# Optimization experiments

Measured on AMD Instinct MI355X. Metric: run time of the kernel, lower is better.

## Reference

```python
import jax, jax.numpy as jnp
import numpy as np
import math

S, B, HID = 1024, 2, 2048
NH, KVH, HDIM = 16, 4, 128
FFN, E, TOPK = 4096, 8, 2
CAP_F = 1.0
Q_PER_KV = NH // KVH
GROUP = (Q_PER_KV + 2) * HDIM
QKV_SIZE = KVH * GROUP
T = S * B
CAPACITY = max(4, int(math.ceil(TOPK * CAP_F * T / E)))
EPS = 1.1920929e-07


def _xavier(key, shape, fan_in, fan_out):
    lim = math.sqrt(6.0 / (fan_in + fan_out))
    return jax.random.uniform(key, shape, jnp.float32, -lim, lim)


def setup_inputs() -> dict:
    key = jax.random.key(0)
    ks = jax.random.split(key, 8)
    return {
        'hidden_states': jax.random.normal(ks[0], (S, B, HID), jnp.float32),
        'ln1_w': jnp.ones((HID,), jnp.float32),
        'ln1_b': jnp.zeros((HID,), jnp.float32),
        'qkv_w': _xavier(ks[1], (QKV_SIZE, HID), HID, QKV_SIZE),
        'proj_w': _xavier(ks[2], (HID, NH * HDIM), NH * HDIM, HID),
        'ln2_w': jnp.ones((HID,), jnp.float32),
        'ln2_b': jnp.zeros((HID,), jnp.float32),
        'gate_w': _xavier(ks[3], (HID, E), HID, E),
        'w1': _xavier(ks[4], (E, HID, FFN), HID, FFN),  # expert fc1 [E, HID, FFN]
        'w2': _xavier(ks[5], (E, FFN, HID), FFN, HID),  # expert fc2 [E, FFN, HID]
    }


def _layer_norm(x, w, b):
    mu = x.mean(-1, keepdims=True)
    var = ((x - mu) ** 2).mean(-1, keepdims=True)
    return (x - mu) * jax.lax.rsqrt(var + 1e-5) * w + b


def _attention(hs, ln1_w, ln1_b, qkv_w, proj_w):
    ln1 = _layer_norm(hs, ln1_w, ln1_b)
    qkv = jnp.einsum('sbh,oh->sbo', ln1, qkv_w)
    qkv = qkv.reshape(S, B, KVH, GROUP)
    q_dim = Q_PER_KV * HDIM
    q = qkv[..., :q_dim].reshape(S, B, NH, HDIM)
    k = qkv[..., q_dim:q_dim + HDIM]          # [S,B,KVH,HDIM]
    v = qkv[..., q_dim + HDIM:]               # [S,B,KVH,HDIM]
    # batch-first, GQA expand kv heads
    q_bf = q.transpose(1, 0, 2, 3)                         # [B,S,NH,HDIM]
    k_bf = jnp.repeat(k.transpose(1, 0, 2, 3), Q_PER_KV, axis=2)
    v_bf = jnp.repeat(v.transpose(1, 0, 2, 3), Q_PER_KV, axis=2)
    scale = 1.0 / math.sqrt(HDIM)
    scores = jnp.einsum('bqhd,bkhd->bhqk', q_bf, k_bf) * scale
    causal = jnp.tril(jnp.ones((S, S), bool))
    scores = jnp.where(causal, scores, jnp.finfo(scores.dtype).min)
    attn = jax.nn.softmax(scores, axis=-1)
    out = jnp.einsum('bhqk,bkhd->bqhd', attn, v_bf)        # [B,S,NH,HDIM]
    out_sp = out.transpose(1, 0, 2, 3).reshape(S, B, NH * HDIM)
    return jnp.einsum('sbo,ho->sbh', out_sp, proj_w)


def _moe(x, gate_w, w1, w2):
    # x: [T, HID]; deterministic DeepSpeed-style top-2 gating with capacity drop
    logits = jnp.einsum('th,he->te', x, gate_w)
    gates = jax.nn.softmax(logits, axis=-1)
    idx1 = jnp.argmax(gates, axis=-1)
    mask1 = jax.nn.one_hot(idx1, E, dtype=jnp.int32)
    logits2 = jnp.where(mask1.astype(bool), jnp.finfo(logits.dtype).min, logits)
    idx2 = jnp.argmax(logits2, axis=-1)
    mask2 = jax.nn.one_hot(idx2, E, dtype=jnp.int32)
    loc1 = jnp.cumsum(mask1, axis=0) - mask1                 # position within expert
    loc2 = jnp.cumsum(mask2, axis=0) - mask2 + mask1.sum(axis=0, keepdims=True)
    mask1 = mask1 * (loc1 < CAPACITY)
    mask2 = mask2 * (loc2 < CAPACITY)
    m1f = mask1.astype(gates.dtype)
    m2f = mask2.astype(gates.dtype)
    g1 = (gates * m1f).sum(-1)
    g2 = (gates * m2f).sum(-1)
    denom = jnp.maximum(g1 + g2, EPS)
    g1, g2 = g1 / denom, g2 / denom
    p1 = (loc1 * mask1).sum(-1)
    p2 = (loc2 * mask2).sum(-1)
    c1 = (g1[:, None] * m1f)[:, :, None] * jax.nn.one_hot(p1, CAPACITY, dtype=gates.dtype)[:, None, :]
    c2 = (g2[:, None] * m2f)[:, :, None] * jax.nn.one_hot(p2, CAPACITY, dtype=gates.dtype)[:, None, :]
    combine = c1 + c2                                        # [T,E,C]
    dispatch = (combine > 0).astype(x.dtype)
    xe = jnp.einsum('tec,th->ech', dispatch, x)              # [E,C,HID]
    h = jax.nn.gelu(jnp.einsum('ech,ehf->ecf', xe, w1), approximate=False)
    eo = jnp.einsum('ecf,efh->ech', h, w2)                   # [E,C,HID]
    return jnp.einsum('tec,ech->th', combine, eo)


def reference(hidden_states, ln1_w, ln1_b, qkv_w, proj_w, ln2_w, ln2_b, gate_w, w1, w2):
    h1 = hidden_states + _attention(hidden_states, ln1_w, ln1_b, qkv_w, proj_w)
    ln2 = _layer_norm(h1, ln2_w, ln2_b)
    moe_out = _moe(ln2.reshape(T, HID), gate_w, w1, w2).reshape(S, B, HID)
    return h1 + moe_out
```

## Files before the change

### kernel.cpp

```cpp
#include <hip/hip_runtime.h>
#include <math.h>

#define S_LEN 1024
#define BATCH 2
#define HIDN  2048
#define NHEAD 16
#define KVHN  4
#define HDIM  128
#define FFND  4096
#define NEXP  8
#define CAPC  512
#define TTOK  2048
#define QKVSZ 3072
#define GRP   768

#define BM  128
#define BKS 32
#define BKM 64
#define LDT 40

typedef float           f32x4 __attribute__((ext_vector_type(4)));
typedef __bf16          bf16x8 __attribute__((ext_vector_type(8)));
typedef unsigned short  u16x8 __attribute__((ext_vector_type(8)));
typedef unsigned short  u16x4 __attribute__((ext_vector_type(4)));

static __device__ __forceinline__ unsigned short f2bf(float f) {
  unsigned int u = __builtin_bit_cast(unsigned int, f);
  u += 0x7FFFu + ((u >> 16) & 1u);
  return (unsigned short)(u >> 16);
}
static __device__ __forceinline__ float bf2f(unsigned short h) {
  unsigned int u = ((unsigned int)h) << 16;
  return __builtin_bit_cast(float, u);
}
static __device__ __forceinline__ bf16x8 ldbf8(const unsigned short* p) {
  return __builtin_bit_cast(bf16x8, *(const u16x8*)p);
}
static __device__ __forceinline__ f32x4 mfma16(bf16x8 a, bf16x8 b, f32x4 c) {
  return __builtin_amdgcn_mfma_f32_16x16x32_bf16(a, b, c, 0, 0, 0);
}
static __device__ __forceinline__ void gl_lds16(const unsigned short* g, unsigned short* l) {
  __builtin_amdgcn_global_load_lds(
      (const __attribute__((address_space(1))) unsigned int*)g,
      (__attribute__((address_space(3))) unsigned int*)l, 16, 0, 0);
}

__global__ __launch_bounds__(256) void ln_kernel(
    const float* __restrict__ X, const float* __restrict__ W, const float* __restrict__ Bi,
    unsigned short* __restrict__ Yh, unsigned short* __restrict__ Yl, float* __restrict__ Yf) {
  __shared__ float red[256];
  int t = blockIdx.x, tid = threadIdx.x;
  const float* row = X + (size_t)t * HIDN;
  float x[8];
  {
    float4 a = *(const float4*)(row + tid * 8);
    float4 b = *(const float4*)(row + tid * 8 + 4);
    x[0]=a.x; x[1]=a.y; x[2]=a.z; x[3]=a.w; x[4]=b.x; x[5]=b.y; x[6]=b.z; x[7]=b.w;
  }
  float s = 0.f;
#pragma unroll
  for (int j = 0; j < 8; j++) s += x[j];
  red[tid] = s; __syncthreads();
  for (int o = 128; o > 0; o >>= 1) { if (tid < o) red[tid] += red[tid + o]; __syncthreads(); }
  float mu = red[0] * (1.0f / HIDN);
  __syncthreads();
  float ss = 0.f;
#pragma unroll
  for (int j = 0; j < 8; j++) { float d = x[j] - mu; ss += d * d; }
  red[tid] = ss; __syncthreads();
  for (int o = 128; o > 0; o >>= 1) { if (tid < o) red[tid] += red[tid + o]; __syncthreads(); }
  float var = red[0] * (1.0f / HIDN);
  float rstd = 1.0f / sqrtf(var + 1e-5f);
#pragma unroll
  for (int j = 0; j < 8; j++) {
    int hh = tid * 8 + j;
    float y = (x[j] - mu) * rstd * W[hh] + Bi[hh];
    size_t idx = (size_t)t * HIDN + hh;
    if (Yf) Yf[idx] = y;
    unsigned short hv = f2bf(y);
    Yh[idx] = hv;
    if (Yl) Yl[idx] = f2bf(y - bf2f(hv));
  }
}

__global__ __launch_bounds__(256) void wsplit(const float* __restrict__ W,
    unsigned short* __restrict__ Wh, unsigned short* __restrict__ Wl) {
  size_t i = ((size_t)blockIdx.x * 256 + threadIdx.x) * 8;
  float4 a = *(const float4*)(W + i);
  float4 b = *(const float4*)(W + i + 4);
  float v[8] = {a.x, a.y, a.z, a.w, b.x, b.y, b.z, b.w};
  u16x8 hv, lv;
#pragma unroll
  for (int j = 0; j < 8; j++) {
    unsigned short h = f2bf(v[j]);
    hv[j] = h; lv[j] = f2bf(v[j] - bf2f(h));
  }
  *(u16x8*)(Wh + i) = hv;
  *(u16x8*)(Wl + i) = lv;
}

__global__ __launch_bounds__(256) void tconv(const float* __restrict__ W,
    unsigned short* __restrict__ Wt, int K, int N) {
  __shared__ unsigned short T[64][72];
  int z = blockIdx.z;
  const float* Wz = W + (size_t)z * K * N;
  unsigned short* Oz = Wt + (size_t)z * N * K;
  int k0 = blockIdx.y * 64, n0 = blockIdx.x * 64;
  int tid = threadIdx.x;
  int kr = (tid >> 4) << 1, n4 = (tid & 15) << 2;
#pragma unroll
  for (int i = 0; i < 2; i++) {
    int k = kr + i * 32;
    float4 a = *(const float4*)(Wz + (size_t)(k0 + k) * N + n0 + n4);
    float4 b = *(const float4*)(Wz + (size_t)(k0 + k + 1) * N + n0 + n4);
    float av[4] = {a.x, a.y, a.z, a.w};
    float bv[4] = {b.x, b.y, b.z, b.w};
#pragma unroll
    for (int j = 0; j < 4; j++) {
      unsigned int pk = (unsigned int)f2bf(av[j]) | ((unsigned int)f2bf(bv[j]) << 16);
      *(unsigned int*)&T[n4 + j][k] = pk;
    }
  }
  __syncthreads();
  int nr = tid >> 3, c = (tid & 7) << 3;
#pragma unroll
  for (int r = 0; r < 2; r++) {
    int n = nr + r * 32;
    u16x8 v = *(const u16x8*)&T[n][c];
    *(u16x8*)(Oz + (size_t)(n0 + n) * K + k0 + c) = v;
  }
}

__global__ __launch_bounds__(256) void gemm_x3s(
    const unsigned short* __restrict__ Ah, const unsigned short* __restrict__ Al,
    const unsigned short* __restrict__ Bh, const unsigned short* __restrict__ Bl,
    float* __restrict__ Cp, int M, int N, int K2, int ldk) {
  __shared__ __align__(16) unsigned short sAh[2][4096], sAl[2][4096], sBh[2][4096], sBl[2][4096];
  int tid = threadIdx.x;
  int nbm = M >> 7, nbn = N >> 7, per = nbm * nbn;
  int cpx = gridDim.x >> 3;
  int bid = blockIdx.x;
  int l = (bid & 7) * cpx + (bid >> 3);
  int kh = l / per;
  int r = l % per;
  int nb = r / nbm, mb = r % nbm;
  int m0 = mb * BM, n0 = nb * BM;
  size_t ko = (size_t)kh * K2;
  int wv = tid >> 6, lane = tid & 63;
  int wr = wv >> 1, wc = wv & 1;
  int lm = lane & 15, lk = lane >> 4;
  f32x4 acc[4][4];
#pragma unroll
  for (int mi = 0; mi < 4; mi++)
#pragma unroll
    for (int ni = 0; ni < 4; ni++) { acc[mi][ni][0]=0.f; acc[mi][ni][1]=0.f; acc[mi][ni][2]=0.f; acc[mi][ni][3]=0.f; }
  int ri = lane >> 2, ccx = lane & 3;
  int swze = (ccx ^ ((ri >> 1) & 3)) * 8;
  int g0 = wv * 2, g1 = g0 + 1;
  const unsigned short* pah0 = Ah + (size_t)(m0 + g0 * 16 + ri) * ldk + ko + swze;
  const unsigned short* pah1 = Ah + (size_t)(m0 + g1 * 16 + ri) * ldk + ko + swze;
  const unsigned short* pal0 = Al + (size_t)(m0 + g0 * 16 + ri) * ldk + ko + swze;
  const unsigned short* pal1 = Al + (size_t)(m0 + g1 * 16 + ri) * ldk + ko + swze;
  const unsigned short* pbh0 = Bh + (size_t)(n0 + g0 * 16 + ri) * ldk + ko + swze;
  const unsigned short* pbh1 = Bh + (size_t)(n0 + g1 * 16 + ri) * ldk + ko + swze;
  const unsigned short* pbl0 = Bl + (size_t)(n0 + g0 * 16 + ri) * ldk + ko + swze;
  const unsigned short* pbl1 = Bl + (size_t)(n0 + g1 * 16 + ri) * ldk + ko + swze;
  int d0 = g0 * 512, d1 = g1 * 512;
  auto stage = [&](int buf, int ks) {
    gl_lds16(pah0 + ks, &sAh[buf][d0]); gl_lds16(pah1 + ks, &sAh[buf][d1]);
    gl_lds16(pal0 + ks, &sAl[buf][d0]); gl_lds16(pal1 + ks, &sAl[buf][d1]);
    gl_lds16(pbh0 + ks, &sBh[buf][d0]); gl_lds16(pbh1 + ks, &sBh[buf][d1]);
    gl_lds16(pbl0 + ks, &sBl[buf][d0]); gl_lds16(pbl1 + ks, &sBl[buf][d1]);
  };
  int nt = K2 / BKS;
  stage(0, 0);
  stage(1, BKS);
  int sa = (lk ^ ((lm >> 1) & 3)) * 8;
  for (int t = 0; t < nt; t++) {
    if (t + 1 < nt) { asm volatile("s_waitcnt vmcnt(8)" ::: "memory"); }
    else            { asm volatile("s_waitcnt vmcnt(0)" ::: "memory"); }
    __builtin_amdgcn_sched_barrier(0);
    __builtin_amdgcn_s_barrier();
    int cur = t & 1;
    bf16x8 fah[4], fal[4], fbh[4], fbl[4];
#pragma unroll
    for (int mi = 0; mi < 4; mi++) {
      int ro = (wr * 64 + mi * 16 + lm) * 32 + sa;
      fah[mi] = ldbf8(&sAh[cur][ro]); fal[mi] = ldbf8(&sAl[cur][ro]);
    }
#pragma unroll
    for (int ni = 0; ni < 4; ni++) {
      int ro = (wc * 64 + ni * 16 + lm) * 32 + sa;
      fbh[ni] = ldbf8(&sBh[cur][ro]); fbl[ni] = ldbf8(&sBl[cur][ro]);
    }
#pragma unroll
    for (int mi = 0; mi < 4; mi++)
#pragma unroll
      for (int ni = 0; ni < 4; ni++) {
        acc[mi][ni] = mfma16(fah[mi], fbh[ni], acc[mi][ni]);
        acc[mi][ni] = mfma16(fal[mi], fbh[ni], acc[mi][ni]);
        acc[mi][ni] = mfma16(fah[mi], fbl[ni], acc[mi][ni]);
      }
    __builtin_amdgcn_s_barrier();
    if (t + 2 < nt) stage(cur, (t + 2) * BKS);
  }
  float* Cslab = Cp + (size_t)kh * M * N;
#pragma unroll
  for (int mi = 0; mi < 4; mi++)
#pragma unroll
    for (int ni = 0; ni < 4; ni++)
#pragma unroll
      for (int rr = 0; rr < 4; rr++) {
        int row = m0 + wr * 64 + mi * 16 + lk * 4 + rr;
        int col = n0 + wc * 64 + ni * 16 + lm;
        Cslab[(size_t)row * N + col] = acc[mi][ni][rr];
      }
}

template<int GELU, int SPLITK>
__global__ __launch_bounds__(256) void gemm_moe(
    const unsigned short* __restrict__ A, const unsigned short* __restrict__ Bt,
    void* __restrict__ Cp, int M, int N, int K, int ld) {
  __shared__ __align__(16) unsigned short sA[2][8192], sB[2][8192];
  int tid = threadIdx.x;
  int nbm = M >> 7, nbn = N >> 7, per = nbm * nbn;
  int cpx = gridDim.x >> 3;
  int bid = blockIdx.x;
  int l = (bid & 7) * cpx + (bid >> 3);
  int z = l / per;
  int r = l % per;
  int nb = r / nbm, mb = r % nbm;
  int m0 = mb * BM, n0 = nb * BM;
  const unsigned short* Az;
  const unsigned short* Bz;
  if (SPLITK) {
    int e = z >> 1, kh = z & 1;
    Az = A + (size_t)e * M * ld + (size_t)kh * K;
    Bz = Bt + (size_t)e * N * ld + (size_t)kh * K;
  } else {
    Az = A + (size_t)z * M * ld;
    Bz = Bt + (size_t)z * N * ld;
  }
  int wv = tid >> 6, lane = tid & 63;
  int wr = wv >> 1, wc = wv & 1;
  int lm = lane & 15, lk = lane >> 4;
  f32x4 acc[4][4];
#pragma unroll
  for (int mi = 0; mi < 4; mi++)
#pragma unroll
    for (int ni = 0; ni < 4; ni++) { acc[mi][ni][0]=0.f; acc[mi][ni][1]=0.f; acc[mi][ni][2]=0.f; acc[mi][ni][3]=0.f; }
  int ri = lane >> 3, cc8 = lane & 7;
  int swze = (cc8 ^ ri) * 8;
  const unsigned short* pa[4];
  const unsigned short* pb[4];
#pragma unroll
  for (int j = 0; j < 4; j++) {
    int g = wv * 4 + j;
    pa[j] = Az + (size_t)(m0 + g * 8 + ri) * ld + swze;
    pb[j] = Bz + (size_t)(n0 + g * 8 + ri) * ld + swze;
  }
  int dbase = wv * 4 * 512;
  auto stage = [&](int buf, int ks) {
#pragma unroll
    for (int j = 0; j < 4; j++) {
      gl_lds16(pa[j] + ks, &sA[buf][dbase + j * 512]);
      gl_lds16(pb[j] + ks, &sB[buf][dbase + j * 512]);
    }
  };
  int nt = K / BKM;
  stage(0, 0);
  stage(1, BKM);
  int sw = lm & 7;
  for (int t = 0; t < nt; t++) {
    if (t + 1 < nt) { asm volatile("s_waitcnt vmcnt(8)" ::: "memory"); }
    else            { asm volatile("s_waitcnt vmcnt(0)" ::: "memory"); }
    __builtin_amdgcn_sched_barrier(0);
    __builtin_amdgcn_s_barrier();
    int cur = t & 1;
#pragma unroll
    for (int h = 0; h < 2; h++) {
      int kc = lk + h * 4;
      int sa = ((kc ^ sw)) * 8;
      bf16x8 fa[4], fb[4];
#pragma unroll
      for (int mi = 0; mi < 4; mi++) fa[mi] = ldbf8(&sA[cur][(wr * 64 + mi * 16 + lm) * 64 + sa]);
#pragma unroll
      for (int ni = 0; ni < 4; ni++) fb[ni] = ldbf8(&sB[cur][(wc * 64 + ni * 16 + lm) * 64 + sa]);
#pragma unroll
      for (int mi = 0; mi < 4; mi++)
#pragma unroll
        for (int ni = 0; ni < 4; ni++)
          acc[mi][ni] = mfma16(fa[mi], fb[ni], acc[mi][ni]);
    }
    __builtin_amdgcn_s_barrier();
    if (t + 2 < nt) stage(cur, (t + 2) * BKM);
  }
#pragma unroll
  for (int mi = 0; mi < 4; mi++)
#pragma unroll
    for (int ni = 0; ni < 4; ni++)
#pragma unroll
      for (int rr = 0; rr < 4; rr++) {
        int row = m0 + wr * 64 + mi * 16 + lk * 4 + rr;
        int col = n0 + wc * 64 + ni * 16 + lm;
        size_t idx = (size_t)z * M * N + (size_t)row * N + col;
        float v = acc[mi][ni][rr];
        if (GELU) {
          float gv = 0.5f * v * (1.0f + erff(v * 0.70710678118654752f));
          ((unsigned short*)Cp)[idx] = f2bf(gv);
        } else {
          ((float*)Cp)[idx] = v;
        }
      }
}

__global__ __launch_bounds__(256) void h1comb(
    const float* __restrict__ hs, const float* __restrict__ p, float* __restrict__ h1) {
  size_t i = ((size_t)blockIdx.x * 256 + threadIdx.x) * 8;
  const float* p0 = p + i;
  const float* p1 = p + (size_t)TTOK * HIDN + i;
#pragma unroll
  for (int j = 0; j < 8; j += 4) {
    float4 a = *(const float4*)(hs + i + j);
    float4 b = *(const float4*)(p0 + j);
    float4 c = *(const float4*)(p1 + j);
    float4 o;
    o.x = a.x + b.x + c.x; o.y = a.y + b.y + c.y;
    o.z = a.z + b.z + c.z; o.w = a.w + b.w + c.w;
    *(float4*)(h1 + i + j) = o;
  }
}

__global__ __launch_bounds__(256) void repack_kernel(
    const float* __restrict__ qkvp,
    unsigned short* __restrict__ Qh, unsigned short* __restrict__ Ql,
    unsigned short* __restrict__ Kh, unsigned short* __restrict__ Kl,
    unsigned short* __restrict__ Vh, unsigned short* __restrict__ Vl) {
  int t = blockIdx.x; int s = t / BATCH, b = t % BATCH;
  const float* row0 = qkvp + (size_t)t * QKVSZ;
  const float* row1 = row0 + (size_t)TTOK * QKVSZ;
  int tid = threadIdx.x;
  for (int idx = tid; idx < 2048; idx += 256) {
    int hh = idx >> 7, d = idx & 127;
    int o_in = (hh >> 2) * GRP + (hh & 3) * 128 + d;
    float val = row0[o_in] + row1[o_in];
    unsigned short hv = f2bf(val), lv = f2bf(val - bf2f(hv));
    size_t o = ((size_t)(b * NHEAD + hh) * S_LEN + s) * HDIM + d;
    Qh[o] = hv; Ql[o] = lv;
  }
  for (int idx = tid; idx < 512; idx += 256) {
    int g = idx >> 7, d = idx & 127;
    int o_in = g * GRP + 512 + d;
    float val = row0[o_in] + row1[o_in];
    unsigned short hv = f2bf(val), lv = f2bf(val - bf2f(hv));
    size_t o = ((size_t)(b * KVHN + g) * S_LEN + s) * HDIM + d;
    Kh[o] = hv; Kl[o] = lv;
  }
  for (int idx = tid; idx < 512; idx += 256) {
    int g = idx >> 7, d = idx & 127;
    int o_in = g * GRP + 640 + d;
    float val = row0[o_in] + row1[o_in];
    unsigned short hv = f2bf(val), lv = f2bf(val - bf2f(hv));
    size_t o = ((size_t)(b * KVHN + g) * HDIM + d) * S_LEN + s;
    Vh[o] = hv; Vl[o] = lv;
  }
}

__global__ __launch_bounds__(256) void attn4(
    const unsigned short* __restrict__ Qh, const unsigned short* __restrict__ Ql,
    const unsigned short* __restrict__ Kh, const unsigned short* __restrict__ Kl,
    const unsigned short* __restrict__ Vh, const unsigned short* __restrict__ Vl,
    unsigned short* __restrict__ Oh, unsigned short* __restrict__ Ol) {
  __shared__ __align__(16) unsigned short sK[2][2][32 * 128];
  __shared__ __align__(16) unsigned short Ph[4][2][16 * LDT], Pl[4][2][16 * LDT];
  int qt = blockIdx.x, g = blockIdx.y, b = blockIdx.z;
  int tid = threadIdx.x, wv = tid >> 6, lane = tid & 63;
  int lm = lane & 15, lk = lane >> 4;
  int hh = g * 4 + wv;
  int q0 = qt * 16;
  const float scale = 0.08838834764831845f;
  int r0 = wv * 4 + (lane >> 4);
  int c16 = lane & 15;
  int dsw = (c16 * 8) ^ ((r0 & 7) << 3);
  const unsigned short* kbh = Kh + (size_t)((b * KVHN + g) * S_LEN) * HDIM;
  const unsigned short* kbl = Kl + (size_t)((b * KVHN + g) * S_LEN) * HDIM;
  auto stageK = [&](int buf, int k0) {
    unsigned short* dh = &sK[buf][0][0];
    unsigned short* dl = &sK[buf][1][0];
    gl_lds16(kbh + (size_t)(k0 + r0) * HDIM + dsw,      dh + wv * 512);
    gl_lds16(kbh + (size_t)(k0 + r0 + 16) * HDIM + dsw, dh + 2048 + wv * 512);
    gl_lds16(kbl + (size_t)(k0 + r0) * HDIM + dsw,      dl + wv * 512);
    gl_lds16(kbl + (size_t)(k0 + r0 + 16) * HDIM + dsw, dl + 2048 + wv * 512);
  };
  bf16x8 qfh[4], qfl[4];
  {
    size_t qb = ((size_t)(b * NHEAD + hh) * S_LEN + q0 + lm) * HDIM + lk * 8;
#pragma unroll
    for (int dc = 0; dc < 4; dc++) {
      qfh[dc] = ldbf8(Qh + qb + dc * 32);
      qfl[dc] = ldbf8(Ql + qb + dc * 32);
    }
  }
  f32x4 accO[8];
#pragma unroll
  for (int dt = 0; dt < 8; dt++) { accO[dt][0]=0.f; accO[dt][1]=0.f; accO[dt][2]=0.f; accO[dt][3]=0.f; }
  float mrun = -3.4e38f, lrun = 0.f;
  int nch = (q0 + 47) >> 5;
  stageK(0, 0);
  asm volatile("s_waitcnt vmcnt(0)" ::: "memory");
  __syncthreads();
  int cur = 0;
  for (int ck = 0; ck < nch; ck++) {
    int k0 = ck * 32;
    if (ck + 1 < nch) stageK(cur ^ 1, k0 + 32);
    f32x4 sc[2];
    sc[0][0]=0.f; sc[0][1]=0.f; sc[0][2]=0.f; sc[0][3]=0.f;
    sc[1][0]=0.f; sc[1][1]=0.f; sc[1][2]=0.f; sc[1][3]=0.f;
#pragma unroll
    for (int t2 = 0; t2 < 2; t2++) {
      int row = t2 * 16 + lm;
#pragma unroll
      for (int dc = 0; dc < 4; dc++) {
        int ce = (dc * 32 + lk * 8) ^ ((row & 7) << 3);
        bf16x8 kfh = ldbf8(&sK[cur][0][row * 128 + ce]);
        bf16x8 kfl = ldbf8(&sK[cur][1][row * 128 + ce]);
        sc[t2] = mfma16(kfh, qfh[dc], sc[t2]);
        sc[t2] = mfma16(kfl, qfh[dc], sc[t2]);
        sc[t2] = mfma16(kfh, qfl[dc], sc[t2]);
      }
    }
    float pv[8];
    float pmax = -3.4e38f;
#pragma unroll
    for (int t2 = 0; t2 < 2; t2++)
#pragma unroll
      for (int rr = 0; rr < 4; rr++) {
        int key = k0 + t2 * 16 + lk * 4 + rr;
        float sv = sc[t2][rr] * scale;
        if (key > q0 + lm) sv = -3.4e38f;
        pv[t2 * 4 + rr] = sv;
        pmax = fmaxf(pmax, sv);
      }
    pmax = fmaxf(pmax, __shfl_xor(pmax, 16));
    pmax = fmaxf(pmax, __shfl_xor(pmax, 32));
    float mnew = fmaxf(mrun, pmax);
    float fsc = expf(mrun - mnew);
    float psum = 0.f;
#pragma unroll
    for (int j = 0; j < 8; j++) { pv[j] = expf(pv[j] - mnew); psum += pv[j]; }
    psum = psum + __shfl_xor(psum, 16);
    psum = psum + __shfl_xor(psum, 32);
    lrun = lrun * fsc + psum;
#pragma unroll
    for (int dt = 0; dt < 8; dt++)
#pragma unroll
      for (int rr = 0; rr < 4; rr++) accO[dt][rr] *= fsc;
    int pb = ck & 1;
#pragma unroll
    for (int t2 = 0; t2 < 2; t2++) {
      u16x4 wh, wl;
#pragma unroll
      for (int rr = 0; rr < 4; rr++) {
        float p = pv[t2 * 4 + rr];
        unsigned short hv = f2bf(p);
        wh[rr] = hv; wl[rr] = f2bf(p - bf2f(hv));
      }
      int ad = lm * LDT + t2 * 16 + lk * 4;
      *(u16x4*)&Ph[wv][pb][ad] = wh;
      *(u16x4*)&Pl[wv][pb][ad] = wl;
    }
    bf16x8 pfh = ldbf8(&Ph[wv][pb][lm * LDT + lk * 8]);
    bf16x8 pfl = ldbf8(&Pl[wv][pb][lm * LDT + lk * 8]);
#pragma unroll
    for (int dt = 0; dt < 8; dt++) {
      size_t vo = ((size_t)((b * KVHN + g) * HDIM + dt * 16 + lm)) * S_LEN + k0 + lk * 8;
      bf16x8 vfh = ldbf8(Vh + vo);
      bf16x8 vfl = ldbf8(Vl + vo);
      accO[dt] = mfma16(vfh, pfh, accO[dt]);
      accO[dt] = mfma16(vfl, pfh, accO[dt]);
      accO[dt] = mfma16(vfh, pfl, accO[dt]);
    }
    mrun = mnew;
    asm volatile("s_waitcnt vmcnt(0)" ::: "memory");
    __syncthreads();
    cur ^= 1;
  }
  float inv = 1.0f / lrun;
#pragma unroll
  for (int dt = 0; dt < 8; dt++)
#pragma unroll
    for (int rr = 0; rr < 4; rr++) {
      float o = accO[dt][rr] * inv;
      int d = dt * 16 + lk * 4 + rr;
      int srow = q0 + lm;
      size_t idx = ((size_t)(srow * BATCH + b)) * HIDN + hh * HDIM + d;
      unsigned short hv = f2bf(o);
      Oh[idx] = hv; Ol[idx] = f2bf(o - bf2f(hv));
    }
}

__global__ __launch_bounds__(256) void gate_logits_kernel(
    const float* __restrict__ X, const float* __restrict__ GW, float* __restrict__ L) {
  __shared__ float red[256][8];
  int t = blockIdx.x, tid = threadIdx.x;
  const float* x = X + (size_t)t * HIDN + tid * 8;
  float acc[8] = {0.f,0.f,0.f,0.f,0.f,0.f,0.f,0.f};
#pragma unroll
  for (int j = 0; j < 8; j++) {
    float xv = x[j];
    const float* gp = GW + (size_t)(tid * 8 + j) * NEXP;
    float4 g0 = *(const float4*)gp;
    float4 g1 = *(const float4*)(gp + 4);
    acc[0] += xv * g0.x; acc[1] += xv * g0.y; acc[2] += xv * g0.z; acc[3] += xv * g0.w;
    acc[4] += xv * g1.x; acc[5] += xv * g1.y; acc[6] += xv * g1.z; acc[7] += xv * g1.w;
  }
#pragma unroll
  for (int k = 0; k < 8; k++) red[tid][k] = acc[k];
  __syncthreads();
  for (int o = 128; o > 0; o >>= 1) {
    if (tid < o) {
#pragma unroll
      for (int k = 0; k < 8; k++) red[tid][k] += red[tid + o][k];
    }
    __syncthreads();
  }
  if (tid < 8) L[(size_t)t * NEXP + tid] = red[0][tid];
}

__global__ __launch_bounds__(1024) void routing_kernel(
    const float* __restrict__ L, int* __restrict__ slot_token,
    int* __restrict__ tE1, int* __restrict__ tP1, float* __restrict__ tG1,
    int* __restrict__ tE2, int* __restrict__ tP2, float* __restrict__ tG2) {
  __shared__ unsigned int sc[1024][8];
  __shared__ unsigned int stot[8];
  int i = threadIdx.x;
  for (int j = i; j < NEXP * CAPC; j += 1024) slot_token[j] = -1;

  int e1[2], e2[2]; float g1[2], g2[2];
  unsigned int v[8] = {0,0,0,0,0,0,0,0};
#pragma unroll
  for (int u = 0; u < 2; u++) {
    int t = 2 * i + u;
    float l[8];
    float m = -3.4e38f;
#pragma unroll
    for (int e = 0; e < 8; e++) { l[e] = L[(size_t)t * NEXP + e]; m = fmaxf(m, l[e]); }
    float ex[8]; float se = 0.f;
#pragma unroll
    for (int e = 0; e < 8; e++) { ex[e] = expf(l[e] - m); se += ex[e]; }
    int b1 = 0; float bv = l[0];
    for (int e = 1; e < 8; e++) if (l[e] > bv) { bv = l[e]; b1 = e; }
    int b2 = -1; float bv2 = 0.f;
    for (int e = 0; e < 8; e++) {
      if (e == b1) continue;
      if (b2 < 0 || l[e] > bv2) { b2 = e; bv2 = l[e]; }
    }
    e1[u] = b1; e2[u] = b2;
    g1[u] = ex[b1] / se; g2[u] = ex[b2] / se;
    v[b1 >> 1] += 1u << ((b1 & 1) * 16);
    v[4 + (b2 >> 1)] += 1u << ((b2 & 1) * 16);
  }
  unsigned int cur[8];
#pragma unroll
  for (int k = 0; k < 8; k++) cur[k] = v[k];
  for (int off = 1; off < 1024; off <<= 1) {
#pragma unroll
    for (int k = 0; k < 8; k++) sc[i][k] = cur[k];
    __syncthreads();
    if (i >= off) {
#pragma unroll
      for (int k = 0; k < 8; k++) cur[k] += sc[i - off][k];
    }
    __syncthreads();
  }
  if (i == 1023) {
#pragma unroll
    for (int k = 0; k < 8; k++) stot[k] = cur[k];
  }
  __syncthreads();
  unsigned int excl[8];
#pragma unroll
  for (int k = 0; k < 8; k++) excl[k] = cur[k] - v[k];

#pragma unroll
  for (int u = 0; u < 2; u++) {
    int t = 2 * i + u;
    int a1 = e1[u], a2 = e2[u];
    int loc1 = (int)((excl[a1 >> 1] >> ((a1 & 1) * 16)) & 0xFFFFu);
    int loc2 = (int)((excl[4 + (a2 >> 1)] >> ((a2 & 1) * 16)) & 0xFFFFu);
    if (u == 1) {
      if (a1 == e1[0]) loc1 += 1;
      if (a2 == e2[0]) loc2 += 1;
    }
    loc2 += (int)((stot[a2 >> 1] >> ((a2 & 1) * 16)) & 0xFFFFu);
    bool k1 = loc1 < CAPC, k2 = loc2 < CAPC;
    float G1 = k1 ? g1[u] : 0.f, G2 = k2 ? g2[u] : 0.f;
    float den = fmaxf(G1 + G2, 1.1920929e-07f);
    G1 /= den; G2 /= den;
    tE1[t] = a1; tP1[t] = k1 ? loc1 : 0; tG1[t] = G1;
    tE2[t] = a2; tP2[t] = k2 ? loc2 : 0; tG2[t] = G2;
    if (k1) slot_token[a1 * CAPC + loc1] = t;
    if (k2) slot_token[a2 * CAPC + loc2] = t;
  }
}

__global__ __launch_bounds__(256) void gather_kernel(
    const int* __restrict__ slot_token, const unsigned short* __restrict__ Xb,
    unsigned short* __restrict__ XE) {
  int slot = blockIdx.x;
  int t = slot_token[slot];
  unsigned short* dst = XE + (size_t)slot * HIDN + threadIdx.x * 8;
  if (t >= 0) {
    *(u16x8*)dst = *(const u16x8*)(Xb + (size_t)t * HIDN + threadIdx.x * 8);
  } else {
    u16x8 zz = {0,0,0,0,0,0,0,0};
    *(u16x8*)dst = zz;
  }
}

__global__ __launch_bounds__(256) void combine_kernel(
    const float* __restrict__ h1, const float* __restrict__ eo2,
    const int* __restrict__ tE1, const int* __restrict__ tP1, const float* __restrict__ tG1,
    const int* __restrict__ tE2, const int* __restrict__ tP2, const float* __restrict__ tG2,
    float* __restrict__ outp) {
  int t = blockIdx.x, tid = threadIdx.x;
  float G1 = tG1[t], G2 = tG2[t];
  size_t MN = (size_t)CAPC * HIDN;
  size_t b1 = ((size_t)tE1[t] * 2) * MN + (size_t)tP1[t] * HIDN;
  size_t b2 = ((size_t)tE2[t] * 2) * MN + (size_t)tP2[t] * HIDN;
  size_t rowo = (size_t)t * HIDN;
  int c = tid * 8;
#pragma unroll
  for (int j = 0; j < 8; j += 4) {
    float4 hv  = *(const float4*)(h1 + rowo + c + j);
    float4 e1a = *(const float4*)(eo2 + b1 + c + j);
    float4 e1b = *(const float4*)(eo2 + b1 + MN + c + j);
    float4 e2a = *(const float4*)(eo2 + b2 + c + j);
    float4 e2b = *(const float4*)(eo2 + b2 + MN + c + j);
    float4 o;
    o.x = hv.x + G1 * (e1a.x + e1b.x) + G2 * (e2a.x + e2b.x);
    o.y = hv.y + G1 * (e1a.y + e1b.y) + G2 * (e2a.y + e2b.y);
    o.z = hv.z + G1 * (e1a.z + e1b.z) + G2 * (e2a.z + e2b.z);
    o.w = hv.w + G1 * (e1a.w + e1b.w) + G2 * (e2a.w + e2b.w);
    *(float4*)(outp + rowo + c + j) = o;
  }
}

extern "C" void kernel_launch(void* const* d_in, const int* in_sizes, int n_in,
                              void* d_out, int out_size, void* d_ws, size_t ws_size,
                              hipStream_t stream) {
  const float* hs    = (const float*)d_in[0];
  const float* ln1w  = (const float*)d_in[1];
  const float* ln1b  = (const float*)d_in[2];
  const float* qkvw  = (const float*)d_in[3];
  const float* projw = (const float*)d_in[4];
  const float* ln2w  = (const float*)d_in[5];
  const float* ln2b  = (const float*)d_in[6];
  const float* gatew = (const float*)d_in[7];
  const float* w1    = (const float*)d_in[8];
  const float* w2    = (const float*)d_in[9];
  float* outp = (float*)d_out;

  char* base = (char*)d_ws;
  size_t off = 0;
  auto alloc = [&](size_t bytes) -> void* {
    void* r = base + off;
    off = (off + bytes + 255) & ~(size_t)255;
    return r;
  };
  unsigned short* ln1h = (unsigned short*)alloc((size_t)TTOK * HIDN * 2);
  unsigned short* ln1l = (unsigned short*)alloc((size_t)TTOK * HIDN * 2);
  float* qkvp = (float*)alloc((size_t)2 * TTOK * QKVSZ * 4);
  unsigned short* Qh = (unsigned short*)alloc((size_t)BATCH * NHEAD * S_LEN * HDIM * 2);
  unsigned short* Ql = (unsigned short*)alloc((size_t)BATCH * NHEAD * S_LEN * HDIM * 2);
  unsigned short* Kh = (unsigned short*)alloc((size_t)BATCH * KVHN * S_LEN * HDIM * 2);
  unsigned short* Kl = (unsigned short*)alloc((size_t)BATCH * KVHN * S_LEN * HDIM * 2);
  unsigned short* Vh = (unsigned short*)alloc((size_t)BATCH * KVHN * S_LEN * HDIM * 2);
  unsigned short* Vl = (unsigned short*)alloc((size_t)BATCH * KVHN * S_LEN * HDIM * 2);
  unsigned short* oh = (unsigned short*)alloc((size_t)TTOK * HIDN * 2);
  unsigned short* ol = (unsigned short*)alloc((size_t)TTOK * HIDN * 2);
  float* h1p = (float*)alloc((size_t)2 * TTOK * HIDN * 4);
  float* h1 = (float*)alloc((size_t)TTOK * HIDN * 4);
  float* xf = (float*)alloc((size_t)TTOK * HIDN * 4);
  unsigned short* xb = (unsigned short*)alloc((size_t)TTOK * HIDN * 2);
  float* logits = (float*)alloc((size_t)TTOK * NEXP * 4);
  int* slot = (int*)alloc((size_t)NEXP * CAPC * 4);
  int* tE1 = (int*)alloc((size_t)TTOK * 4);
  int* tP1 = (int*)alloc((size_t)TTOK * 4);
  int* tE2 = (int*)alloc((size_t)TTOK * 4);
  int* tP2 = (int*)alloc((size_t)TTOK * 4);
  float* tG1 = (float*)alloc((size_t)TTOK * 4);
  float* tG2 = (float*)alloc((size_t)TTOK * 4);
  unsigned short* xe = (unsigned short*)alloc((size_t)NEXP * CAPC * HIDN * 2);
  unsigned short* hmid = (unsigned short*)alloc((size_t)NEXP * CAPC * FFND * 2);
  float* eo2 = (float*)alloc((size_t)NEXP * 2 * CAPC * HIDN * 4);
  unsigned short* qwh = (unsigned short*)alloc((size_t)QKVSZ * HIDN * 2);
  unsigned short* qwl = (unsigned short*)alloc((size_t)QKVSZ * HIDN * 2);
  unsigned short* pwh = (unsigned short*)alloc((size_t)HIDN * HIDN * 2);
  unsigned short* pwl = (unsigned short*)alloc((size_t)HIDN * HIDN * 2);
  unsigned short* wt = (unsigned short*)alloc((size_t)NEXP * FFND * HIDN * 2);
  (void)ws_size; (void)in_sizes; (void)n_in; (void)out_size;

  ln_kernel<<<TTOK, 256, 0, stream>>>(hs, ln1w, ln1b, ln1h, ln1l, nullptr);
  wsplit<<<(QKVSZ * HIDN) / 2048, 256, 0, stream>>>(qkvw, qwh, qwl);
  wsplit<<<(HIDN * HIDN) / 2048, 256, 0, stream>>>(projw, pwh, pwl);
  gemm_x3s<<<dim3((QKVSZ / BM) * (TTOK / BM) * 2), 256, 0, stream>>>(
      ln1h, ln1l, qwh, qwl, qkvp, TTOK, QKVSZ, HIDN / 2, HIDN);
  repack_kernel<<<TTOK, 256, 0, stream>>>(qkvp, Qh, Ql, Kh, Kl, Vh, Vl);
  attn4<<<dim3(S_LEN / 16, KVHN, BATCH), 256, 0, stream>>>(Qh, Ql, Kh, Kl, Vh, Vl, oh, ol);
  gemm_x3s<<<dim3((HIDN / BM) * (TTOK / BM) * 2), 256, 0, stream>>>(
      oh, ol, pwh, pwl, h1p, TTOK, HIDN, HIDN / 2, HIDN);
  h1comb<<<(TTOK * HIDN) / 2048, 256, 0, stream>>>(hs, h1p, h1);
  ln_kernel<<<TTOK, 256, 0, stream>>>(h1, ln2w, ln2b, xb, nullptr, xf);
  gate_logits_kernel<<<TTOK, 256, 0, stream>>>(xf, gatew, logits);
  routing_kernel<<<1, 1024, 0, stream>>>(logits, slot, tE1, tP1, tG1, tE2, tP2, tG2);
  gather_kernel<<<NEXP * CAPC, 256, 0, stream>>>(slot, xb, xe);
  tconv<<<dim3(FFND / 64, HIDN / 64, NEXP), 256, 0, stream>>>(w1, wt, HIDN, FFND);
  gemm_moe<1, 0><<<dim3((FFND / BM) * (CAPC / BM) * NEXP), 256, 0, stream>>>(
      xe, wt, (void*)hmid, CAPC, FFND, HIDN, HIDN);
  tconv<<<dim3(HIDN / 64, FFND / 64, NEXP), 256, 0, stream>>>(w2, wt, FFND, HIDN);
  gemm_moe<0, 1><<<dim3((HIDN / BM) * (CAPC / BM) * NEXP * 2), 256, 0, stream>>>(
      hmid, wt, (void*)eo2, CAPC, HIDN, FFND / 2, FFND);
  combine_kernel<<<TTOK, 256, 0, stream>>>(h1, eo2, tE1, tP1, tG1, tE2, tP2, tG2, outp);
}
```

Measured before the change: 789.8 us.

## Fuse fp32 expert-weight transpose/convert into MoE GEMM B-tile loading

After: 706.1 us. -10.6%, faster.

```diff
diff --git a/kernel.cpp b/kernel.cpp
--- a/kernel.cpp
+++ b/kernel.cpp
@@ -97,38 +97,6 @@
   }
   *(u16x8*)(Wh + i) = hv;
   *(u16x8*)(Wl + i) = lv;
-}
-
-__global__ __launch_bounds__(256) void tconv(const float* __restrict__ W,
-    unsigned short* __restrict__ Wt, int K, int N) {
-  __shared__ unsigned short T[64][72];
-  int z = blockIdx.z;
-  const float* Wz = W + (size_t)z * K * N;
-  unsigned short* Oz = Wt + (size_t)z * N * K;
-  int k0 = blockIdx.y * 64, n0 = blockIdx.x * 64;
-  int tid = threadIdx.x;
-  int kr = (tid >> 4) << 1, n4 = (tid & 15) << 2;
-#pragma unroll
-  for (int i = 0; i < 2; i++) {
-    int k = kr + i * 32;
-    float4 a = *(const float4*)(Wz + (size_t)(k0 + k) * N + n0 + n4);
-    float4 b = *(const float4*)(Wz + (size_t)(k0 + k + 1) * N + n0 + n4);
-    float av[4] = {a.x, a.y, a.z, a.w};
-    float bv[4] = {b.x, b.y, b.z, b.w};
-#pragma unroll
-    for (int j = 0; j < 4; j++) {
-      unsigned int pk = (unsigned int)f2bf(av[j]) | ((unsigned int)f2bf(bv[j]) << 16);
-      *(unsigned int*)&T[n4 + j][k] = pk;
-    }
-  }
-  __syncthreads();
-  int nr = tid >> 3, c = (tid & 7) << 3;
-#pragma unroll
-  for (int r = 0; r < 2; r++) {
-    int n = nr + r * 32;
-    u16x8 v = *(const u16x8*)&T[n][c];
-    *(u16x8*)(Oz + (size_t)(n0 + n) * K + k0 + c) = v;
-  }
 }
 
 __global__ __launch_bounds__(256) void gemm_x3s(
@@ -218,9 +186,9 @@
 }
 
 template<int GELU, int SPLITK>
-__global__ __launch_bounds__(256) void gemm_moe(
-    const unsigned short* __restrict__ A, const unsigned short* __restrict__ Bt,
-    void* __restrict__ Cp, int M, int N, int K, int ld) {
+__global__ __launch_bounds__(256) void gemm_moeF(
+    const unsigned short* __restrict__ A, const float* __restrict__ Bsrc,
+    void* __restrict__ Cp, int M, int N, int K, int ldA, int ldB) {
   __shared__ __align__(16) unsigned short sA[2][8192], sB[2][8192];
   int tid = threadIdx.x;
   int nbm = M >> 7, nbn = N >> 7, per = nbm * nbn;
@@ -232,14 +200,14 @@
   int nb = r / nbm, mb = r % nbm;
   int m0 = mb * BM, n0 = nb * BM;
   const unsigned short* Az;
-  const unsigned short* Bz;
+  const float* Bz;
   if (SPLITK) {
     int e = z >> 1, kh = z & 1;
-    Az = A + (size_t)e * M * ld + (size_t)kh * K;
-    Bz = Bt + (size_t)e * N * ld + (size_t)kh * K;
+    Az = A + (size_t)e * M * ldA + (size_t)kh * K;
+    Bz = Bsrc + (size_t)e * (2 * (size_t)K) * ldB + (size_t)kh * K * ldB;
   } else {
-    Az = A + (size_t)z * M * ld;
-    Bz = Bt + (size_t)z * N * ld;
+    Az = A + (size_t)z * M * ldA;
+    Bz = Bsrc + (size_t)z * (size_t)K * ldB;
   }
   int wv = tid >> 6, lane = tid & 63;
   int wr = wv >> 1, wc = wv & 1;
@@ -250,37 +218,68 @@
 #pragma unroll
     for (int ni = 0; ni < 4; ni++) { acc[mi][ni][0]=0.f; acc[mi][ni][1]=0.f; acc[mi][ni][2]=0.f; acc[mi][ni][3]=0.f; }
   int ri = lane >> 3, cc8 = lane & 7;
-  int swze = (cc8 ^ ri) * 8;
+  int swzeA = (cc8 ^ ri) * 8;
   const unsigned short* pa[4];
-  const unsigned short* pb[4];
-#pragma unroll
-  for (int j = 0; j < 4; j++) {
-    int g = wv * 4 + j;
-    pa[j] = Az + (size_t)(m0 + g * 8 + ri) * ld + swze;
-    pb[j] = Bz + (size_t)(n0 + g * 8 + ri) * ld + swze;
-  }
-  int dbase = wv * 4 * 512;
-  auto stage = [&](int buf, int ks) {
+#pragma unroll
+  for (int j = 0; j < 4; j++)
+    pa[j] = Az + (size_t)(m0 + (wv * 4 + j) * 8 + ri) * ldA + swzeA;
+  int dbaseA = wv * 4 * 512;
+  auto stageA = [&](int buf, int ks) {
+#pragma unroll
+    for (int j = 0; j < 4; j++)
+      gl_lds16(pa[j] + ks, &sA[buf][dbaseA + j * 512]);
+  };
+  int tq = tid & 31;
+  int kpb = (tid >> 5) * 4;
+  float bs[32];
+  auto issueB = [&](int ks) {
 #pragma unroll
     for (int j = 0; j < 4; j++) {
-      gl_lds16(pa[j] + ks, &sA[buf][dbase + j * 512]);
-      gl_lds16(pb[j] + ks, &sB[buf][dbase + j * 512]);
+      int kk = (kpb + j) * 2;
+#pragma unroll
+      for (int rr = 0; rr < 2; rr++)
+#pragma unroll
+        for (int i = 0; i < 4; i++)
+          bs[j * 8 + rr * 4 + i] = Bz[(size_t)(ks + kk + rr) * ldB + n0 + i * 32 + tq];
+    }
+  };
+  auto cvtwriteB = [&](int buf) {
+    unsigned short* dB = &sB[buf][0];
+#pragma unroll
+    for (int j = 0; j < 4; j++) {
+      int kp = kpb + j;
+      int cpb = kp >> 2;
+      int wpos = (kp & 3) * 2;
+#pragma unroll
+      for (int i = 0; i < 4; i++) {
+        int n = i * 32 + tq;
+        unsigned int pk = (unsigned int)f2bf(bs[j * 8 + i]) |
+                          ((unsigned int)f2bf(bs[j * 8 + 4 + i]) << 16);
+        int elem = n * 64 + ((cpb ^ (n & 7)) * 8) + wpos;
+        *(unsigned int*)&dB[elem] = pk;
+      }
     }
   };
   int nt = K / BKM;
-  stage(0, 0);
-  stage(1, BKM);
+  stageA(0, 0);
+  issueB(0);
+  asm volatile("s_waitcnt vmcnt(0)" ::: "memory");
+  __builtin_amdgcn_sched_barrier(0);
+  cvtwriteB(0);
+  __syncthreads();
   int sw = lm & 7;
   for (int t = 0; t < nt; t++) {
-    if (t + 1 < nt) { asm volatile("s_waitcnt vmcnt(8)" ::: "memory"); }
-    else            { asm volatile("s_waitcnt vmcnt(0)" ::: "memory"); }
-    __builtin_amdgcn_sched_barrier(0);
-    __builtin_amdgcn_s_barrier();
     int cur = t & 1;
+    bool more = (t + 1 < nt);
+    if (more) {
+      stageA(cur ^ 1, (t + 1) * BKM);
+      issueB((t + 1) * BKM);
+      __builtin_amdgcn_sched_barrier(0);
+    }
 #pragma unroll
     for (int h = 0; h < 2; h++) {
       int kc = lk + h * 4;
-      int sa = ((kc ^ sw)) * 8;
+      int sa = (kc ^ sw) * 8;
       bf16x8 fa[4], fb[4];
 #pragma unroll
       for (int mi = 0; mi < 4; mi++) fa[mi] = ldbf8(&sA[cur][(wr * 64 + mi * 16 + lm) * 64 + sa]);
@@ -292,8 +291,13 @@
         for (int ni = 0; ni < 4; ni++)
           acc[mi][ni] = mfma16(fa[mi], fb[ni], acc[mi][ni]);
     }
-    __builtin_amdgcn_s_barrier();
-    if (t + 2 < nt) stage(cur, (t + 2) * BKM);
+    if (more) {
+      asm volatile("s_waitcnt vmcnt(0)" ::: "memory");
+      __builtin_amdgcn_sched_barrier(0);
+      __syncthreads();
+      cvtwriteB(cur ^ 1);
+      __syncthreads();
+    }
   }
 #pragma unroll
   for (int mi = 0; mi < 4; mi++)
@@ -698,7 +702,6 @@
   unsigned short* qwl = (unsigned short*)alloc((size_t)QKVSZ * HIDN * 2);
   unsigned short* pwh = (unsigned short*)alloc((size_t)HIDN * HIDN * 2);
   unsigned short* pwl = (unsigned short*)alloc((size_t)HIDN * HIDN * 2);
-  unsigned short* wt = (unsigned short*)alloc((size_t)NEXP * FFND * HIDN * 2);
   (void)ws_size; (void)in_sizes; (void)n_in; (void)out_size;
 
   ln_kernel<<<TTOK, 256, 0, stream>>>(hs, ln1w, ln1b, ln1h, ln1l, nullptr);
@@ -715,11 +718,9 @@
   gate_logits_kernel<<<TTOK, 256, 0, stream>>>(xf, gatew, logits);
   routing_kernel<<<1, 1024, 0, stream>>>(logits, slot, tE1, tP1, tG1, tE2, tP2, tG2);
   gather_kernel<<<NEXP * CAPC, 256, 0, stream>>>(slot, xb, xe);
-  tconv<<<dim3(FFND / 64, HIDN / 64, NEXP), 256, 0, stream>>>(w1, wt, HIDN, FFND);
-  gemm_moe<1, 0><<<dim3((FFND / BM) * (CAPC / BM) * NEXP), 256, 0, stream>>>(
-      xe, wt, (void*)hmid, CAPC, FFND, HIDN, HIDN);
-  tconv<<<dim3(HIDN / 64, FFND / 64, NEXP), 256, 0, stream>>>(w2, wt, FFND, HIDN);
-  gemm_moe<0, 1><<<dim3((HIDN / BM) * (CAPC / BM) * NEXP * 2), 256, 0, stream>>>(
-      hmid, wt, (void*)eo2, CAPC, HIDN, FFND / 2, FFND);
+  gemm_moeF<1, 0><<<dim3((FFND / BM) * (CAPC / BM) * NEXP), 256, 0, stream>>>(
+      xe, w1, (void*)hmid, CAPC, FFND, HIDN, HIDN, FFND);
+  gemm_moeF<0, 1><<<dim3((HIDN / BM) * (CAPC / BM) * NEXP * 2), 256, 0, stream>>>(
+      hmid, w2, (void*)eo2, CAPC, HIDN, FFND / 2, FFND, HIDN);
   combine_kernel<<<TTOK, 256, 0, stream>>>(h1, eo2, tE1, tP1, tG1, tE2, tP2, tG2, outp);
 }
```
